# Optimization experiments

Measured on AMD Instinct MI355X. Metric: run time of the kernel, lower is better.

Reference implementation:

```python
import jax, jax.numpy as jnp
import numpy as np

B, S, D, H = 2, 2048, 1024, 16
DK = D // H


def setup_inputs() -> dict:
    key = jax.random.key(0)
    ks = jax.random.split(key, 7)
    q = jax.random.normal(ks[0], (B, S, D), dtype=jnp.float32)
    k = jax.random.normal(ks[1], (B, S, D), dtype=jnp.float32)
    v = jax.random.normal(ks[2], (B, S, D), dtype=jnp.float32)
    # causal mask (1 = keep, 0 = mask) broadcast over batch/heads
    mask = jnp.tril(jnp.ones((S, S), dtype=jnp.int32))[None, None, :, :]
    scale = 1.0 / np.sqrt(DK)
    W_q = jax.random.normal(ks[3], (D, D), dtype=jnp.float32) * 0.02
    W_k = jax.random.normal(ks[4], (D, D), dtype=jnp.float32) * 0.02
    W_v = jax.random.normal(ks[5], (D, D), dtype=jnp.float32) * 0.02
    W_o = jax.random.normal(ks[6], (D, D), dtype=jnp.float32) * 0.02
    return {"q": q, "k": k, "v": v, "mask": mask,
            "W_q": W_q, "W_k": W_k, "W_v": W_v, "W_o": W_o}


def _split_heads(x):
    # [B, S, D] -> [B, H, S, DK]
    b, s, _ = x.shape
    return x.reshape(b, s, H, DK).transpose(0, 2, 1, 3)


def reference(q, k, v, mask, W_q, W_k, W_v, W_o):
    # nn.Linear(bias=False): y = x @ W.T
    qh = _split_heads(q @ W_q.T)
    kh = _split_heads(k @ W_k.T)
    vh = _split_heads(v @ W_v.T)
    scores = jnp.einsum("bhqd,bhkd->bhqk", qh, kh) / np.sqrt(DK)
    scores = jnp.where(mask == 0, jnp.float32(-1e9), scores)
    attn = jax.nn.softmax(scores, axis=-1)  # dropout p=0 -> identity
    out = jnp.einsum("bhqk,bhkd->bhqd", attn, vh)
    out = out.transpose(0, 2, 1, 3).reshape(q.shape[0], q.shape[1], D)
    return out @ W_o.T
```

## Files before the change

### kernel.cpp

```cpp
#include <hip/hip_runtime.h>
#include <stdint.h>
#include <stddef.h>

typedef __bf16 bf16;
typedef __attribute__((ext_vector_type(4))) __bf16 bf16x4;
typedef __attribute__((ext_vector_type(8))) __bf16 bf16x8;
typedef __attribute__((ext_vector_type(4))) float floatx4;

#define NB 2
#define NS 2048
#define ND 1024
#define NH 16
#define NDK 64
#define NBH (NB*NH)
#define NBS (NB*NS)

__device__ inline void gl2lds16(const void* g, void* l) {
  __builtin_amdgcn_global_load_lds(
      (const __attribute__((address_space(1))) uint32_t*)(const uint32_t*)g,
      (__attribute__((address_space(3))) uint32_t*)(uint32_t*)l,
      16, 0, 0);
}

__global__ __launch_bounds__(256)
void convert_w3(const float* __restrict__ Wq, const float* __restrict__ Wk,
                const float* __restrict__ Wv, bf16* __restrict__ Wb)
{
  const int z = blockIdx.y;
  const float* src = (z == 0) ? Wq : (z == 1) ? Wk : Wv;
  bf16* dst = Wb + (size_t)z * (ND * ND);
  const size_t off = ((size_t)blockIdx.x * 256 + threadIdx.x) * 32;
#pragma unroll
  for (int c = 0; c < 2; c++) {
    bf16x8 o[2];
#pragma unroll
    for (int h = 0; h < 2; h++) {
      const float4 a = *(const float4*)(src + off + c * 16 + h * 8);
      const float4 b = *(const float4*)(src + off + c * 16 + h * 8 + 4);
      o[h][0] = (bf16)a.x; o[h][1] = (bf16)a.y; o[h][2] = (bf16)a.z; o[h][3] = (bf16)a.w;
      o[h][4] = (bf16)b.x; o[h][5] = (bf16)b.y; o[h][6] = (bf16)b.z; o[h][7] = (bf16)b.w;
    }
    *(bf16x8*)(dst + off + c * 16) = o[0];
    *(bf16x8*)(dst + off + c * 16 + 8) = o[1];
  }
}

__global__ __launch_bounds__(256)
void convert_w1(const float* __restrict__ src, bf16* __restrict__ dst)
{
  const size_t off = ((size_t)blockIdx.x * 256 + threadIdx.x) * 32;
#pragma unroll
  for (int c = 0; c < 2; c++) {
    bf16x8 o[2];
#pragma unroll
    for (int h = 0; h < 2; h++) {
      const float4 a = *(const float4*)(src + off + c * 16 + h * 8);
      const float4 b = *(const float4*)(src + off + c * 16 + h * 8 + 4);
      o[h][0] = (bf16)a.x; o[h][1] = (bf16)a.y; o[h][2] = (bf16)a.z; o[h][3] = (bf16)a.w;
      o[h][4] = (bf16)b.x; o[h][5] = (bf16)b.y; o[h][6] = (bf16)b.z; o[h][7] = (bf16)b.w;
    }
    *(bf16x8*)(dst + off + c * 16) = o[0];
    *(bf16x8*)(dst + off + c * 16 + 8) = o[1];
  }
}

__global__ __launch_bounds__(256)
void proj_gemm(const float* __restrict__ q, const float* __restrict__ k,
               const float* __restrict__ v, const bf16* __restrict__ Wb,
               bf16* __restrict__ Qh, bf16* __restrict__ Kh,
               bf16* __restrict__ Vt)
{
  const int z = blockIdx.y, bx = blockIdx.x;
  const int tid = threadIdx.x;
  const int wave = tid >> 6, lane = tid & 63;
  const int quad = lane >> 4, l15 = lane & 15;

  const float* X = (z == 0) ? q : (z == 1) ? k : v;
  const bf16* W = Wb + (size_t)z * (ND * ND);
  const int c = bx & 7, r = bx >> 3;
  const int m0 = (c * 4 + (r >> 3)) * 128, n0 = (r & 7) * 128;

  __shared__ bf16 As[128 * 32];
  __shared__ bf16 Bs[128 * 32];

  const int arow = tid >> 3, ach = tid & 7;

  const int wm = (wave >> 1) * 64, wn = (wave & 1) * 64;

  floatx4 acc[4][4];
#pragma unroll
  for (int i = 0; i < 4; i++)
#pragma unroll
    for (int j = 0; j < 4; j++) acc[i][j] = (floatx4)(0.0f);

  float4 ra[4];
  bf16x8 rb[2];

  auto loadA = [&](int kt) {
    const int k0 = kt * 32;
#pragma unroll
    for (int it = 0; it < 4; it++)
      ra[it] = *(const float4*)(X + (size_t)(m0 + it * 32 + arow) * ND + k0 + ach * 4);
  };
  auto loadB = [&](int kt) {
    const int k0 = kt * 32;
#pragma unroll
    for (int it = 0; it < 2; it++) {
      const int lin = it * 256 + tid;
      const int row = lin >> 2, ch = lin & 3;
      rb[it] = *(const bf16x8*)(W + (size_t)(n0 + row) * ND + k0 + ch * 8);
    }
  };

  loadA(0); loadB(0);

  for (int kk = 0; kk < 32; kk++) {
    __syncthreads();
#pragma unroll
    for (int it = 0; it < 4; it++) {
      bf16x4 a;
      a[0] = (bf16)ra[it].x; a[1] = (bf16)ra[it].y;
      a[2] = (bf16)ra[it].z; a[3] = (bf16)ra[it].w;
      *(bf16x4*)(As + (it * 32 + arow) * 32 + ach * 4) = a;
    }
#pragma unroll
    for (int it = 0; it < 2; it++) {
      const int lin = it * 256 + tid;
      const int row = lin >> 2, ch = lin & 3;
      *(bf16x8*)(Bs + row * 32 + ch * 8) = rb[it];
    }
    __syncthreads();
    if (kk + 1 < 32) { loadA(kk + 1); loadB(kk + 1); }

    bf16x8 af[4], bfr[4];
#pragma unroll
    for (int i = 0; i < 4; i++)
      af[i] = *(const bf16x8*)(As + (wm + i * 16 + l15) * 32 + quad * 8);
#pragma unroll
    for (int j = 0; j < 4; j++)
      bfr[j] = *(const bf16x8*)(Bs + (wn + j * 16 + l15) * 32 + quad * 8);
#pragma unroll
    for (int i = 0; i < 4; i++)
#pragma unroll
      for (int j = 0; j < 4; j++)
        acc[i][j] = __builtin_amdgcn_mfma_f32_16x16x32_bf16(af[i], bfr[j],
                                                            acc[i][j], 0, 0, 0);
  }

  bf16* O = (z == 0) ? Qh : (z == 1) ? Kh : Vt;
#pragma unroll
  for (int i = 0; i < 4; i++) {
    const int rowb = m0 + wm + i * 16 + quad * 4;
#pragma unroll
    for (int j = 0; j < 4; j++) {
      const int col = n0 + wn + j * 16 + l15;
#pragma unroll
      for (int rr = 0; rr < 4; rr++) {
        const int row = rowb + rr;
        const bf16 o = (bf16)acc[i][j][rr];
        const int b = row >> 11, s = row & 2047;
        const int h = col >> 6,  dk = col & 63;
        if (z < 2)
          O[(((size_t)(b * NH + h)) * NS + s) * NDK + dk] = o;
        else
          O[(((size_t)(b * NH + h)) * NDK + dk) * NS + s] = o;
      }
    }
  }
}

__global__ __launch_bounds__(256)
void attn_fwd(const bf16* __restrict__ Qh, const bf16* __restrict__ Kh,
              const bf16* __restrict__ Vt, bf16* __restrict__ Ctx)
{
  const int x = blockIdx.x, bh = blockIdx.y;
  const int tid = threadIdx.x, wave = tid >> 6, lane = tid & 63;
  const int quad = lane >> 4, l15 = lane & 15;

  __shared__ bf16 Ks[2][64 * 64];
  __shared__ bf16 Vs[2][64 * 64];
  __shared__ bf16 Ps[4][16 * 64];

  const size_t qkb = (size_t)bh * NS * NDK;
  const size_t vb  = (size_t)bh * NDK * NS;
  const int b = bh >> 4, h = bh & 15;
  const float C = 0.125f * 1.44269504088896f;

  auto stage = [&](int kt, int buf) {
#pragma unroll
    for (int it = 0; it < 2; it++) {
      const int lin = it * 256 + tid;
      const int row = lin >> 3;
      const int chS = (lin & 7) ^ (row & 7);
      gl2lds16(Kh + qkb + (size_t)(kt * 64 + row) * NDK + chS * 8,
               Ks[buf] + lin * 8);
      gl2lds16(Vt + vb + (size_t)row * NS + kt * 64 + chS * 8,
               Vs[buf] + lin * 8);
    }
  };

  for (int ph = 0; ph < 2; ph++) {
    const int qt = ph ? x : 31 - x;
    const int qrow0 = qt * 64 + wave * 16;

    bf16x8 qf0, qf1;
    {
      const bf16* qp = Qh + qkb + (size_t)(qrow0 + l15) * NDK + quad * 8;
      qf0 = *(const bf16x8*)qp;
      qf1 = *(const bf16x8*)(qp + 32);
    }

    float lsum[4] = {0.0f, 0.0f, 0.0f, 0.0f};
    floatx4 oacc[4];
#pragma unroll
    for (int j = 0; j < 4; j++) oacc[j] = (floatx4)(0.0f);

    __syncthreads();
    stage(0, 0);

    for (int kt = 0; kt <= qt; kt++) {
      const int cur = kt & 1;
      __builtin_amdgcn_s_waitcnt(0);
      __syncthreads();
      if (kt < qt) stage(kt + 1, cur ^ 1);

      const bf16* Ksb = Ks[cur];
      const bf16* Vsb = Vs[cur];

      floatx4 sa[4];
#pragma unroll
      for (int jt = 0; jt < 4; jt++) {
        const int rr = jt * 16 + l15;
        const bf16x8 kf0 = *(const bf16x8*)(Ksb + rr * 64 + ((quad ^ (rr & 7)) << 3));
        const bf16x8 kf1 = *(const bf16x8*)(Ksb + rr * 64 + (((4 + quad) ^ (rr & 7)) << 3));
        floatx4 zz = (floatx4)(0.0f);
        zz = __builtin_amdgcn_mfma_f32_16x16x32_bf16(qf0, kf0, zz, 0, 0, 0);
        zz = __builtin_amdgcn_mfma_f32_16x16x32_bf16(qf1, kf1, zz, 0, 0, 0);
        sa[jt] = zz;
      }

      const bool diag = (kt == qt);
#pragma unroll
      for (int jt = 0; jt < 4; jt++) {
        const int col = jt * 16 + l15;
#pragma unroll
        for (int rr = 0; rr < 4; rr++) {
          const int row = quad * 4 + rr;
          float p = exp2f(sa[jt][rr] * C);
          if (diag) p = (kt * 64 + col <= qrow0 + row) ? p : 0.0f;
          lsum[rr] += p;
          Ps[wave][row * 64 + ((((col >> 3) ^ (row & 7))) << 3) + (col & 7)] =
              (bf16)p;
        }
      }

#pragma unroll
      for (int ks = 0; ks < 2; ks++) {
        const bf16x8 pf = *(const bf16x8*)(
            &Ps[wave][l15 * 64 + (((ks * 4 + quad) ^ (l15 & 7)) << 3)]);
#pragma unroll
        for (int jt = 0; jt < 4; jt++) {
          const int rr = jt * 16 + l15;
          const bf16x8 vf = *(const bf16x8*)(
              Vsb + rr * 64 + (((ks * 4 + quad) ^ (rr & 7)) << 3));
          oacc[jt] = __builtin_amdgcn_mfma_f32_16x16x32_bf16(pf, vf,
                                                             oacc[jt], 0, 0, 0);
        }
      }
    }

#pragma unroll
    for (int off = 1; off < 16; off <<= 1)
#pragma unroll
      for (int rr = 0; rr < 4; rr++) lsum[rr] += __shfl_xor(lsum[rr], off, 64);

#pragma unroll
    for (int jt = 0; jt < 4; jt++)
#pragma unroll
      for (int rr = 0; rr < 4; rr++) {
        const int srow = qrow0 + quad * 4 + rr;
        Ctx[((size_t)b * NS + srow) * ND + h * 64 + jt * 16 + l15] =
            (bf16)(oacc[jt][rr] / lsum[rr]);
      }
  }
}

__global__ __launch_bounds__(256)
void out_gemm(const bf16* __restrict__ Ctx, const bf16* __restrict__ WoB,
              float* __restrict__ out)
{
  const int bx = blockIdx.x, tid = threadIdx.x;
  const int wave = tid >> 6, lane = tid & 63;
  const int quad = lane >> 4, l15 = lane & 15;
  const int c = bx & 7, r = bx >> 3;
  const int m0 = (c * 8 + (r >> 3)) * 64, n0 = (r & 7) * 128;
  const int wm = (wave & 1) * 32, wn = (wave >> 1) * 64;

  __shared__ bf16 As[64 * 32];
  __shared__ bf16 Bs[128 * 32];

  const int arow = tid >> 2, ach = tid & 3;

  floatx4 acc[2][4];
#pragma unroll
  for (int i = 0; i < 2; i++)
#pragma unroll
    for (int j = 0; j < 4; j++) acc[i][j] = (floatx4)(0.0f);

  bf16x8 ra;
  bf16x8 rb[2];

  auto loadA = [&](int kt) {
    ra = *(const bf16x8*)(Ctx + (size_t)(m0 + arow) * ND + kt * 32 + ach * 8);
  };
  auto loadB = [&](int kt) {
#pragma unroll
    for (int it = 0; it < 2; it++) {
      const int lin = it * 256 + tid;
      const int row = lin >> 2, ch = lin & 3;
      rb[it] = *(const bf16x8*)(WoB + (size_t)(n0 + row) * ND + kt * 32 + ch * 8);
    }
  };

  loadA(0); loadB(0);

  for (int kk = 0; kk < 32; kk++) {
    __syncthreads();
    *(bf16x8*)(As + arow * 32 + ach * 8) = ra;
#pragma unroll
    for (int it = 0; it < 2; it++) {
      const int lin = it * 256 + tid;
      const int row = lin >> 2, ch = lin & 3;
      *(bf16x8*)(Bs + row * 32 + ch * 8) = rb[it];
    }
    __syncthreads();
    if (kk + 1 < 32) { loadA(kk + 1); loadB(kk + 1); }

    bf16x8 af[2], bfr[4];
#pragma unroll
    for (int i = 0; i < 2; i++)
      af[i] = *(const bf16x8*)(As + (wm + i * 16 + l15) * 32 + quad * 8);
#pragma unroll
    for (int j = 0; j < 4; j++)
      bfr[j] = *(const bf16x8*)(Bs + (wn + j * 16 + l15) * 32 + quad * 8);
#pragma unroll
    for (int i = 0; i < 2; i++)
#pragma unroll
      for (int j = 0; j < 4; j++)
        acc[i][j] = __builtin_amdgcn_mfma_f32_16x16x32_bf16(af[i], bfr[j],
                                                            acc[i][j], 0, 0, 0);
  }

#pragma unroll
  for (int i = 0; i < 2; i++) {
    const int rowb = m0 + wm + i * 16 + quad * 4;
#pragma unroll
    for (int j = 0; j < 4; j++) {
      const int col = n0 + wn + j * 16 + l15;
#pragma unroll
      for (int rr = 0; rr < 4; rr++)
        out[(size_t)(rowb + rr) * ND + col] = acc[i][j][rr];
    }
  }
}

extern "C" void kernel_launch(void* const* d_in, const int* in_sizes, int n_in,
                              void* d_out, int out_size, void* d_ws, size_t ws_size,
                              hipStream_t stream) {
  const float* q  = (const float*)d_in[0];
  const float* k  = (const float*)d_in[1];
  const float* v  = (const float*)d_in[2];
  const float* Wq = (const float*)d_in[4];
  const float* Wk = (const float*)d_in[5];
  const float* Wv = (const float*)d_in[6];
  const float* Wo = (const float*)d_in[7];
  float* out = (float*)d_out;

  const size_t elems = (size_t)NBS * ND;
  bf16* Qh  = (bf16*)d_ws;
  bf16* Kh  = Qh + elems;
  bf16* Vt  = Kh + elems;
  bf16* Ctx = Vt + elems;
  bf16* Wb  = Ctx;
  bf16* WoB = Vt;

  dim3 blk(256);
  convert_w3<<<dim3(128, 3), blk, 0, stream>>>(Wq, Wk, Wv, Wb);
  proj_gemm<<<dim3(256, 3), blk, 0, stream>>>(q, k, v, Wb, Qh, Kh, Vt);
  attn_fwd<<<dim3(16, NBH), blk, 0, stream>>>(Qh, Kh, Vt, Ctx);
  convert_w1<<<dim3(128), blk, 0, stream>>>(Wo, WoB);
  out_gemm<<<dim3(512), blk, 0, stream>>>(Ctx, WoB, out);
}
```

Baseline: 243.0 us.

## Shrink projection GEMM M-tile to 64 and prefetch A two K-steps ahead

The QKV projection GEMM now uses 64x128 output tiles instead of 128x128, which doubles the grid to 512x3 blocks. This is meant to give better occupancy and CU fill on the device. The fp32 A-operand loads are double-buffered in registers (even and odd sets), so global loads for A run two K-steps ahead of the MFMA work and more latency is hidden. The cost is less operand reuse per block, so more global and L2 traffic for the weight tiles, plus extra register pressure.

```diff
diff --git a/kernel.cpp b/kernel.cpp
--- a/kernel.cpp
+++ b/kernel.cpp
@@ -78,78 +78,91 @@
   const float* X = (z == 0) ? q : (z == 1) ? k : v;
   const bf16* W = Wb + (size_t)z * (ND * ND);
   const int c = bx & 7, r = bx >> 3;
-  const int m0 = (c * 4 + (r >> 3)) * 128, n0 = (r & 7) * 128;
-
-  __shared__ bf16 As[128 * 32];
+  const int m0 = (c * 8 + (r >> 3)) * 64, n0 = (r & 7) * 128;
+
+  __shared__ bf16 As[64 * 32];
   __shared__ bf16 Bs[128 * 32];
 
-  const int arow = tid >> 3, ach = tid & 7;
-
-  const int wm = (wave >> 1) * 64, wn = (wave & 1) * 64;
-
-  floatx4 acc[4][4];
-#pragma unroll
-  for (int i = 0; i < 4; i++)
+  const int wm = (wave & 1) * 32, wn = (wave >> 1) * 64;
+
+  floatx4 acc[2][4];
+#pragma unroll
+  for (int i = 0; i < 2; i++)
 #pragma unroll
     for (int j = 0; j < 4; j++) acc[i][j] = (floatx4)(0.0f);
 
-  float4 ra[4];
+  float4 raE[2], raO[2];
   bf16x8 rb[2];
 
-  auto loadA = [&](int kt) {
+  auto loadA = [&](int kt, float4 (&ra)[2]) {
     const int k0 = kt * 32;
 #pragma unroll
-    for (int it = 0; it < 4; it++)
-      ra[it] = *(const float4*)(X + (size_t)(m0 + it * 32 + arow) * ND + k0 + ach * 4);
+    for (int it = 0; it < 2; it++) {
+      const int lin = it * 256 + tid, row = lin >> 3, ch = lin & 7;
+      ra[it] = *(const float4*)(X + (size_t)(m0 + row) * ND + k0 + ch * 4);
+    }
   };
   auto loadB = [&](int kt) {
     const int k0 = kt * 32;
 #pragma unroll
     for (int it = 0; it < 2; it++) {
-      const int lin = it * 256 + tid;
-      const int row = lin >> 2, ch = lin & 3;
+      const int lin = it * 256 + tid, row = lin >> 2, ch = lin & 3;
       rb[it] = *(const bf16x8*)(W + (size_t)(n0 + row) * ND + k0 + ch * 8);
     }
   };
-
-  loadA(0); loadB(0);
-
-  for (int kk = 0; kk < 32; kk++) {
-    __syncthreads();
-#pragma unroll
-    for (int it = 0; it < 4; it++) {
+  auto stageA = [&](float4 (&ra)[2]) {
+#pragma unroll
+    for (int it = 0; it < 2; it++) {
+      const int lin = it * 256 + tid, row = lin >> 3, ch = lin & 7;
       bf16x4 a;
       a[0] = (bf16)ra[it].x; a[1] = (bf16)ra[it].y;
       a[2] = (bf16)ra[it].z; a[3] = (bf16)ra[it].w;
-      *(bf16x4*)(As + (it * 32 + arow) * 32 + ach * 4) = a;
-    }
-#pragma unroll
-    for (int it = 0; it < 2; it++) {
-      const int lin = it * 256 + tid;
-      const int row = lin >> 2, ch = lin & 3;
+      *(bf16x4*)(As + row * 32 + ch * 4) = a;
+    }
+  };
+  auto stageB = [&]() {
+#pragma unroll
+    for (int it = 0; it < 2; it++) {
+      const int lin = it * 256 + tid, row = lin >> 2, ch = lin & 3;
       *(bf16x8*)(Bs + row * 32 + ch * 8) = rb[it];
     }
-    __syncthreads();
-    if (kk + 1 < 32) { loadA(kk + 1); loadB(kk + 1); }
-
-    bf16x8 af[4], bfr[4];
-#pragma unroll
-    for (int i = 0; i < 4; i++)
+  };
+  auto mfma_step = [&]() {
+    bf16x8 af[2], bfr[4];
+#pragma unroll
+    for (int i = 0; i < 2; i++)
       af[i] = *(const bf16x8*)(As + (wm + i * 16 + l15) * 32 + quad * 8);
 #pragma unroll
     for (int j = 0; j < 4; j++)
       bfr[j] = *(const bf16x8*)(Bs + (wn + j * 16 + l15) * 32 + quad * 8);
 #pragma unroll
-    for (int i = 0; i < 4; i++)
+    for (int i = 0; i < 2; i++)
 #pragma unroll
       for (int j = 0; j < 4; j++)
         acc[i][j] = __builtin_amdgcn_mfma_f32_16x16x32_bf16(af[i], bfr[j],
                                                             acc[i][j], 0, 0, 0);
+  };
+
+  loadA(0, raE); loadB(0); loadA(1, raO);
+
+  for (int kk = 0; kk < 32; kk += 2) {
+    __syncthreads();
+    stageA(raE); stageB();
+    __syncthreads();
+    if (kk + 2 < 32) loadA(kk + 2, raE);
+    if (kk + 1 < 32) loadB(kk + 1);
+    mfma_step();
+    __syncthreads();
+    stageA(raO); stageB();
+    __syncthreads();
+    if (kk + 3 < 32) loadA(kk + 3, raO);
+    if (kk + 2 < 32) loadB(kk + 2);
+    mfma_step();
   }
 
   bf16* O = (z == 0) ? Qh : (z == 1) ? Kh : Vt;
 #pragma unroll
-  for (int i = 0; i < 4; i++) {
+  for (int i = 0; i < 2; i++) {
     const int rowb = m0 + wm + i * 16 + quad * 4;
 #pragma unroll
     for (int j = 0; j < 4; j++) {
@@ -386,7 +399,7 @@
 
   dim3 blk(256);
   convert_w3<<<dim3(128, 3), blk, 0, stream>>>(Wq, Wk, Wv, Wb);
-  proj_gemm<<<dim3(256, 3), blk, 0, stream>>>(q, k, v, Wb, Qh, Kh, Vt);
+  proj_gemm<<<dim3(512, 3), blk, 0, stream>>>(q, k, v, Wb, Qh, Kh, Vt);
   attn_fwd<<<dim3(16, NBH), blk, 0, stream>>>(Qh, Kh, Vt, Ctx);
   convert_w1<<<dim3(128), blk, 0, stream>>>(Wo, WoB);
   out_gemm<<<dim3(512), blk, 0, stream>>>(Ctx, WoB, out);
```

New measurement: 247.7 us. About the same (+1.9%).
